# Kernel tuning notes

Hardware: AMD Instinct MI355X
Metric: run time of the kernel (lower is better)

## Reference

```python
import jax, jax.numpy as jnp
import numpy as np

NHEAD = 8
NEG_INF = -1e9
LN_EPS = 1e-5


def setup_inputs() -> dict:
    key = jax.random.key(0)
    ks = jax.random.split(key, 8)
    B, Q, N, C = 2, 256, 16384, 256
    return {
        "queries": jax.random.normal(ks[0], (B, Q, C), jnp.float32),
        "vid_features": jax.random.normal(ks[1], (B, C, N), jnp.float32),
        "vid_mask": jax.random.uniform(ks[2], (B, Q, N), jnp.float32),
        "pos_embed": jax.random.normal(ks[3], (B, C, N), jnp.float32),
        "query_embed": jax.random.normal(ks[4], (B, Q, C), jnp.float32),
        "in_proj_w": jax.random.normal(ks[5], (3 * C, C), jnp.float32) * 0.02,
        "in_proj_b": jnp.zeros((3 * C,), jnp.float32),
        "out_proj_w": jax.random.normal(ks[6], (C, C), jnp.float32) * 0.02,
        "out_proj_b": jnp.zeros((C,), jnp.float32),
        "ln_gamma": jnp.ones((C,), jnp.float32),
        "ln_beta": jnp.zeros((C,), jnp.float32),
    }


def reference(queries, vid_features, vid_mask, pos_embed, query_embed,
              in_proj_w, in_proj_b, out_proj_w, out_proj_b, ln_gamma, ln_beta):
    B, Q, C = queries.shape
    H = NHEAD
    d = C // H

    vf = jnp.transpose(vid_features, (0, 2, 1))   # B N C
    pe = jnp.transpose(pos_embed, (0, 2, 1))      # B N C

    q_in = queries + query_embed                  # with_pos_embed on queries
    k_in = vf + pe                                # with_pos_embed on keys
    v_in = vf

    wq, wk, wv = jnp.split(in_proj_w, 3, axis=0)
    bq, bk, bv = jnp.split(in_proj_b, 3)

    q = (q_in @ wq.T + bq).reshape(B, Q, H, d)
    k = (k_in @ wk.T + bk).reshape(B, -1, H, d)
    v = (v_in @ wv.T + bv).reshape(B, -1, H, d)

    scale = 1.0 / jnp.sqrt(jnp.asarray(d, q.dtype))
    logits = jnp.einsum('bqhd,bnhd->bhqn', q, k) * scale  # B H Q N

    # Hard masking: block keys where mask prob < 0.5; if a query row is
    # fully blocked, fall back to unmasked attention (avoid NaN softmax).
    blocked = vid_mask < 0.5                                 # B Q N
    all_blocked = jnp.all(blocked, axis=-1, keepdims=True)   # B Q 1
    blocked = blocked & jnp.logical_not(all_blocked)
    logits = jnp.where(blocked[:, None, :, :], NEG_INF, logits)

    attn = jax.nn.softmax(logits, axis=-1)
    ctx = jnp.einsum('bhqn,bnhd->bqhd', attn, v).reshape(B, Q, C)
    tgt2 = ctx @ out_proj_w.T + out_proj_b

    # residual + LayerNorm (dropout p=0.0 -> identity)
    x = queries + tgt2
    mu = jnp.mean(x, axis=-1, keepdims=True)
    var = jnp.mean(jnp.square(x - mu), axis=-1, keepdims=True)
    return (x - mu) / jnp.sqrt(var + LN_EPS) * ln_gamma + ln_beta
```

## Files before the change

kernel.cpp:

```cpp
#include <hip/hip_runtime.h>
#include <stdint.h>

#define B_ 2
#define Q_ 256
#define N_ 16384
#define C_ 256
#define H_ 8
#define D_ 32
#define NC_ 32
#define SCALE 0.17677669529663687f

typedef __bf16 bf16x8 __attribute__((ext_vector_type(8)));
typedef float f32x4 __attribute__((ext_vector_type(4)));

__device__ __forceinline__ uint16_t bfbits(float f) {
  union { __bf16 h; uint16_t u; } c;
  c.h = (__bf16)f;
  return c.u;
}
__device__ __forceinline__ uint16_t f2bf(float f) {
  union { float f; uint32_t u; } c; c.f = f;
  uint32_t r = c.u + 0x7FFFu + ((c.u >> 16) & 1u);
  return (uint16_t)(r >> 16);
}
__device__ __forceinline__ uint32_t pk2(float a, float b) {
  return (uint32_t)f2bf(a) | ((uint32_t)f2bf(b) << 16);
}
__device__ __forceinline__ void lgkm0_barrier() {
  __builtin_amdgcn_sched_barrier(0);
  asm volatile("s_waitcnt lgkmcnt(0)" ::: "memory");
  __builtin_amdgcn_sched_barrier(0);
  __builtin_amdgcn_s_barrier();
  __builtin_amdgcn_sched_barrier(0);
}

__global__ __launch_bounds__(256) void prep(const float* __restrict__ inw,
                                            const float* __restrict__ outw,
                                            const float* __restrict__ vm,
                                            uint16_t* __restrict__ wb,
                                            float* __restrict__ woT,
                                            uint32_t* __restrict__ mb) {
  __shared__ __align__(16) char sh[4352];
  const int bid = blockIdx.x;
  const int t = threadIdx.x;
  if (bid < 96) {
    const int i = (bid * 256 + t) * 8;
    const float4 a = *reinterpret_cast<const float4*>(inw + i);
    const float4 b = *reinterpret_cast<const float4*>(inw + i + 4);
    ushort4 lo = {bfbits(a.x), bfbits(a.y), bfbits(a.z), bfbits(a.w)};
    ushort4 hi = {bfbits(b.x), bfbits(b.y), bfbits(b.z), bfbits(b.w)};
    *reinterpret_cast<ushort4*>(wb + i) = lo;
    *reinterpret_cast<ushort4*>(wb + i + 4) = hi;
  } else if (bid < 160) {
    float(*s)[33] = reinterpret_cast<float(*)[33]>(sh);
    const int bb = bid - 96;
    const int bx = bb & 7, by = bb >> 3;
    const int r0 = by * 32, c0 = bx * 32;
    const int tr = t >> 5, tc = t & 31;
#pragma unroll
    for (int k = 0; k < 4; ++k)
      s[tr + 8 * k][tc] = outw[(size_t)(r0 + tr + 8 * k) * 256 + c0 + tc];
    __syncthreads();
#pragma unroll
    for (int k = 0; k < 4; ++k)
      woT[(size_t)(c0 + tr + 8 * k) * 256 + r0 + tc] = s[tc][tr + 8 * k];
  } else {
    uint8_t(*nib)[256] = reinterpret_cast<uint8_t(*)[256]>(sh);
    __shared__ int wcnt[4];
    __shared__ int tot;
    const int bq = bid - 160;
    const float* row = vm + (size_t)bq * N_;
    const int lane = t & 63;
    int cnt = 0;
#pragma unroll
    for (int i = 0; i < 16; ++i) {
      const float4 v = *reinterpret_cast<const float4*>(&row[i * 1024 + 4 * t]);
      const uint32_t nb = (v.x < 0.5f ? 1u : 0u) | (v.y < 0.5f ? 2u : 0u) |
                          (v.z < 0.5f ? 4u : 0u) | (v.w < 0.5f ? 8u : 0u);
      nib[i][t] = (uint8_t)nb;
      cnt += __popc(nb);
    }
    for (int o = 32; o > 0; o >>= 1) cnt += __shfl_down(cnt, o, 64);
    if (lane == 0) wcnt[t >> 6] = cnt;
    __syncthreads();
    if (t == 0) tot = wcnt[0] + wcnt[1] + wcnt[2] + wcnt[3];
    __syncthreads();
    const bool allb = (tot == N_);
    uint32_t* dst = mb + (size_t)bq * 512;
#pragma unroll
    for (int k = 0; k < 2; ++k) {
      const int w = k * 256 + t;
      const int i = w >> 5, tw = w & 31;
      const uint2 u = *reinterpret_cast<const uint2*>(&nib[i][8 * tw]);
      uint32_t y0 = u.x & 0x0F0F0F0Fu; y0 = y0 | (y0 >> 4);
      uint32_t y1 = u.y & 0x0F0F0F0Fu; y1 = y1 | (y1 >> 4);
      const uint32_t word = (y0 & 0xFFu) | (((y0 >> 16) & 0xFFu) << 8) |
                            ((y1 & 0xFFu) << 16) | (((y1 >> 16) & 0xFFu) << 24);
      dst[w] = allb ? 0u : word;
    }
  }
}

__global__ __launch_bounds__(512) void kvqproj(const float* __restrict__ vf,
                                               const float* __restrict__ pe,
                                               const float* __restrict__ queries,
                                               const float* __restrict__ qembed,
                                               const uint16_t* __restrict__ wkv,
                                               const float* __restrict__ bias,
                                               uint16_t* __restrict__ Kb,
                                               uint16_t* __restrict__ Vb,
                                               uint16_t* __restrict__ Qb) {
  __shared__ __align__(16) uint16_t lds[8][64][40];
  const int bid = blockIdx.x;
  const int t = threadIdx.x, wid = t >> 6, lane = t & 63;
  const int g = lane >> 4, c15 = lane & 15;

  if (bid < 1024) {
    const int nb = bid & 511, b = bid >> 9;
    const int n0 = nb * 32;
    const int cin = t >> 1, nh = (t & 1) * 16;
    const int s = cin >> 5, cl = cin & 31;
    const float* Xrow = vf + ((size_t)b * C_ + cin) * N_ + n0 + nh;
    const float* Prow = pe + ((size_t)b * C_ + cin) * N_ + n0 + nh;
    float4 xr4[4], pr4[4];
#pragma unroll
    for (int k = 0; k < 4; ++k) xr4[k] = reinterpret_cast<const float4*>(Xrow)[k];
#pragma unroll
    for (int k = 0; k < 4; ++k) pr4[k] = reinterpret_cast<const float4*>(Prow)[k];
    const float* xf = reinterpret_cast<const float*>(xr4);
    const float* pf = reinterpret_cast<const float*>(pr4);
#pragma unroll
    for (int i = 0; i < 16; ++i) {
      const int n = nh + i;
      const int col = cl ^ (8 * ((n >> 3) & 3));
      lds[s][n][col] = bfbits(xf[i] + pf[i]);
      lds[s][32 + n][col] = bfbits(xf[i]);
    }
    lgkm0_barrier();

    const bool isK = wid < 4;
    const int wc = wid & 3;
    const uint16_t* W = wkv + (isK ? 256 * C_ : 512 * C_);
    f32x4 acc[4][2];
    if (isK) {
#pragma unroll
      for (int cf = 0; cf < 4; ++cf) {
        f32x4 iv;
#pragma unroll
        for (int j = 0; j < 4; ++j) iv[j] = bias[256 + wc * 64 + cf * 16 + 4 * g + j];
        acc[cf][0] = iv;
        acc[cf][1] = iv;
      }
    } else {
#pragma unroll
      for (int cf = 0; cf < 4; ++cf) {
        const float bv = bias[512 + wc * 64 + cf * 16 + c15];
        const f32x4 iv = {bv, bv, bv, bv};
        acc[0][cf] = iv;
        acc[1][cf] = iv;
      }
    }
#pragma unroll
    for (int s8 = 0; s8 < 8; ++s8) {
      bf16x8 Wf[4];
#pragma unroll
      for (int cf = 0; cf < 4; ++cf)
        Wf[cf] = *reinterpret_cast<const bf16x8*>(
            W + (size_t)(wc * 64 + cf * 16 + c15) * C_ + s8 * 32 + g * 8);
      if (isK) {
#pragma unroll
        for (int nf = 0; nf < 2; ++nf) {
          const int r = nf * 16 + c15;
          const bf16x8 Bf = *reinterpret_cast<const bf16x8*>(
              &lds[s8][r][8 * (g ^ ((r >> 3) & 3))]);
#pragma unroll
          for (int cf = 0; cf < 4; ++cf)
            acc[cf][nf] = __builtin_amdgcn_mfma_f32_16x16x32_bf16(Wf[cf], Bf, acc[cf][nf], 0, 0, 0);
        }
      } else {
#pragma unroll
        for (int nf = 0; nf < 2; ++nf) {
          const int r = nf * 16 + c15;
          const bf16x8 Af = *reinterpret_cast<const bf16x8*>(
              &lds[s8][32 + r][8 * (g ^ ((r >> 3) & 3))]);
#pragma unroll
          for (int cf = 0; cf < 4; ++cf)
            acc[nf][cf] = __builtin_amdgcn_mfma_f32_16x16x32_bf16(Af, Wf[cf], acc[nf][cf], 0, 0, 0);
        }
      }
    }
    if (isK) {
      uint16_t* Kp = Kb + (size_t)b * N_ * C_;
#pragma unroll
      for (int cf = 0; cf < 4; ++cf)
#pragma unroll
        for (int nf = 0; nf < 2; ++nf) {
          const f32x4 a = acc[cf][nf];
          uint2 pkv;
          pkv.x = pk2(a[0], a[1]);
          pkv.y = pk2(a[2], a[3]);
          *reinterpret_cast<uint2*>(
              &Kp[(size_t)(n0 + nf * 16 + c15) * C_ + wc * 64 + cf * 16 + 4 * g]) = pkv;
        }
    } else {
      uint16_t* Vp = Vb + (size_t)b * C_ * N_;
#pragma unroll
      for (int nf = 0; nf < 2; ++nf)
#pragma unroll
        for (int cf = 0; cf < 4; ++cf) {
          const f32x4 a = acc[nf][cf];
          uint2 pkv;
          pkv.x = pk2(a[0], a[1]);
          pkv.y = pk2(a[2], a[3]);
          *reinterpret_cast<uint2*>(
              &Vp[(size_t)(wc * 64 + cf * 16 + c15) * N_ + n0 + nf * 16 + 4 * g]) = pkv;
        }
    }
  } else {
    const int qb = bid - 1024;
    const int q0g = qb * 64;
    const int b = q0g >> 8, q0 = q0g & 255;
    const int r = t >> 3, c0 = (t & 7) * 32, s = t & 7;
    const float* Qrow = queries + (size_t)(q0g + r) * C_ + c0;
    const float* Erow = qembed + (size_t)(q0g + r) * C_ + c0;
#pragma unroll
    for (int ph = 0; ph < 2; ++ph) {
      float4 a4[4], e4[4];
#pragma unroll
      for (int k = 0; k < 4; ++k) a4[k] = reinterpret_cast<const float4*>(Qrow + ph * 16)[k];
#pragma unroll
      for (int k = 0; k < 4; ++k) e4[k] = reinterpret_cast<const float4*>(Erow + ph * 16)[k];
      const float* af = reinterpret_cast<const float*>(a4);
      const float* ef = reinterpret_cast<const float*>(e4);
#pragma unroll
      for (int i = 0; i < 16; ++i) {
        const int cl = ph * 16 + i;
        const int col = cl ^ (8 * ((r >> 3) & 3));
        lds[s][r][col] = bfbits(af[i] + ef[i]);
      }
      __builtin_amdgcn_sched_barrier(0);
    }
    lgkm0_barrier();

    const int w = wid;
    f32x4 acc[4][2];
#pragma unroll
    for (int nf = 0; nf < 2; ++nf) {
      const float bv = bias[w * 32 + nf * 16 + c15];
      const f32x4 iv = {bv, bv, bv, bv};
#pragma unroll
      for (int qf = 0; qf < 4; ++qf) acc[qf][nf] = iv;
    }
#pragma unroll
    for (int s8 = 0; s8 < 8; ++s8) {
      bf16x8 Bf[2];
#pragma unroll
      for (int nf = 0; nf < 2; ++nf)
        Bf[nf] = *reinterpret_cast<const bf16x8*>(
            wkv + (size_t)(w * 32 + nf * 16 + c15) * C_ + s8 * 32 + g * 8);
#pragma unroll
      for (int qf = 0; qf < 4; ++qf) {
        const int rr = qf * 16 + c15;
        const bf16x8 Af = *reinterpret_cast<const bf16x8*>(
            &lds[s8][rr][8 * (g ^ ((rr >> 3) & 3))]);
#pragma unroll
        for (int nf = 0; nf < 2; ++nf)
          acc[qf][nf] = __builtin_amdgcn_mfma_f32_16x16x32_bf16(Af, Bf[nf], acc[qf][nf], 0, 0, 0);
      }
    }
#pragma unroll
    for (int qf = 0; qf < 4; ++qf)
#pragma unroll
      for (int nf = 0; nf < 2; ++nf)
#pragma unroll
        for (int j = 0; j < 4; ++j) {
          const int q = q0 + qf * 16 + 4 * g + j;
          const int dk = nf * 16 + c15;
          Qb[((size_t)(b * H_ + w) * Q_ + q) * D_ + dk] = f2bf(acc[qf][nf][j] * SCALE);
        }
  }
}

__global__ __launch_bounds__(512) void attn(const uint16_t* __restrict__ Qb,
                                            const uint16_t* __restrict__ Kb,
                                            const uint16_t* __restrict__ Vb,
                                            const uint32_t* __restrict__ mb,
                                            float* __restrict__ ctx_part,
                                            float* __restrict__ lsum_part) {
  const int bid = blockIdx.x;
  const int nc = bid & 31, h = (bid >> 5) & 7, b = bid >> 8;
  const int t = threadIdx.x, wid = t >> 6, lane = t & 63;
  const int g = lane >> 4, c15 = lane & 15;
  const int qw0 = wid * 32;
  const int nbase = nc * (N_ / NC_);
  constexpr int SS = (N_ / NC_) / 128;

  __shared__ __align__(16) uint16_t kst[2][128][40];
  __shared__ __align__(16) uint16_t vst[2][32][136];
  __shared__ __align__(16) uint16_t plds[8][32][40];

  const uint16_t* Qp = Qb + (size_t)(b * H_ + h) * Q_ * D_;
  bf16x8 qfr[2];
#pragma unroll
  for (int qf = 0; qf < 2; ++qf)
    qfr[qf] = *reinterpret_cast<const bf16x8*>(Qp + (size_t)(qw0 + qf * 16 + c15) * D_ + g * 8);

  f32x4 acc[2][2];
  const f32x4 zero4 = {0.f, 0.f, 0.f, 0.f};
#pragma unroll
  for (int qf = 0; qf < 2; ++qf)
#pragma unroll
    for (int dvf = 0; dvf < 2; ++dvf) acc[qf][dvf] = zero4;
  float lsum[2][4] = {};

  const uint32_t* mrow = mb + (size_t)b * Q_ * (N_ / 32);

  const int krow = t >> 2, kch = t & 3;
  const uint16_t* ksrc = Kb + ((size_t)(b * N_ + nbase + krow)) * C_ + h * D_ + kch * 8;
  const int vrow = t >> 4, vch = t & 15;
  const uint16_t* vsrc = Vb + ((size_t)(b * C_ + h * D_ + vrow)) * N_ + nbase + vch * 8;

  uint4 kreg = *(const uint4*)ksrc;
  uint4 vreg = *(const uint4*)vsrc;

  int cur = 0;
  for (int ss = 0; ss < SS; ++ss) {
    *(uint4*)&kst[cur][krow][kch * 8] = kreg;
    *(uint4*)&vst[cur][vrow][vch * 8] = vreg;
    if (ss < SS - 1) {
      kreg = *(const uint4*)(ksrc + (size_t)(ss + 1) * 128 * C_);
      vreg = *(const uint4*)(vsrc + (ss + 1) * 128);
    }
    lgkm0_barrier();

    const int nstart = nbase + ss * 128;
#pragma unroll
    for (int half = 0; half < 2; ++half) {
      uint32_t mw[2][4][2];
#pragma unroll
      for (int qf = 0; qf < 2; ++qf)
#pragma unroll
        for (int j = 0; j < 4; ++j) {
          const int q = qw0 + qf * 16 + 4 * g + j;
          const uint2 u = *reinterpret_cast<const uint2*>(
              &mrow[(size_t)q * (N_ / 32) + (nstart >> 5) + half * 2]);
          mw[qf][j][0] = u.x;
          mw[qf][j][1] = u.y;
        }
#pragma unroll
      for (int s2 = 0; s2 < 2; ++s2) {
        const int sub = half * 2 + s2;
        const int nl0 = sub * 32;
        bf16x8 kfr[2];
#pragma unroll
        for (int nf = 0; nf < 2; ++nf)
          kfr[nf] = *reinterpret_cast<const bf16x8*>(&kst[cur][nl0 + nf * 16 + c15][g * 8]);
        f32x4 s[2][2];
#pragma unroll
        for (int qf = 0; qf < 2; ++qf)
#pragma unroll
          for (int nf = 0; nf < 2; ++nf)
            s[qf][nf] = __builtin_amdgcn_mfma_f32_16x16x32_bf16(qfr[qf], kfr[nf], zero4, 0, 0, 0);

#pragma unroll
        for (int qf = 0; qf < 2; ++qf) {
#pragma unroll
          for (int j = 0; j < 4; ++j) {
            const uint32_t wmask = mw[qf][j][s2];
#pragma unroll
            for (int nf = 0; nf < 2; ++nf) {
              const int bit = nf * 16 + c15;
              const float p = ((wmask >> bit) & 1u) ? 0.0f : __expf(s[qf][nf][j]);
              lsum[qf][j] += p;
              plds[wid][qf * 16 + 4 * g + j][nf * 16 + c15] = f2bf(p);
            }
          }
        }
        __asm__ volatile("s_waitcnt lgkmcnt(0)" ::: "memory");
#pragma unroll
        for (int qf = 0; qf < 2; ++qf) {
          const bf16x8 pa = *reinterpret_cast<const bf16x8*>(&plds[wid][qf * 16 + c15][g * 8]);
#pragma unroll
          for (int dvf = 0; dvf < 2; ++dvf) {
            const bf16x8 vb =
                *reinterpret_cast<const bf16x8*>(&vst[cur][dvf * 16 + c15][nl0 + g * 8]);
            acc[qf][dvf] = __builtin_amdgcn_mfma_f32_16x16x32_bf16(pa, vb, acc[qf][dvf], 0, 0, 0);
          }
        }
      }
    }
    __builtin_amdgcn_sched_barrier(0);
    cur ^= 1;
  }

#pragma unroll
  for (int qf = 0; qf < 2; ++qf)
#pragma unroll
    for (int j = 0; j < 4; ++j) {
      float v = lsum[qf][j];
      v += __shfl_xor(v, 1, 64);
      v += __shfl_xor(v, 2, 64);
      v += __shfl_xor(v, 4, 64);
      v += __shfl_xor(v, 8, 64);
      lsum[qf][j] = v;
    }

  float* cp = ctx_part + ((size_t)(b * H_ + h) * NC_ + nc) * Q_ * D_;
#pragma unroll
  for (int qf = 0; qf < 2; ++qf)
#pragma unroll
    for (int dvf = 0; dvf < 2; ++dvf)
#pragma unroll
      for (int j = 0; j < 4; ++j) {
        const int q = qw0 + qf * 16 + 4 * g + j;
        cp[(size_t)q * D_ + dvf * 16 + c15] = acc[qf][dvf][j];
      }
  if (c15 == 0) {
    float* lp = lsum_part + ((size_t)(b * H_ + h) * NC_ + nc) * Q_;
#pragma unroll
    for (int qf = 0; qf < 2; ++qf)
#pragma unroll
      for (int j = 0; j < 4; ++j) lp[qw0 + qf * 16 + 4 * g + j] = lsum[qf][j];
  }
}

__global__ __launch_bounds__(256) void epilogue(const float* __restrict__ ctx_part,
                                                const float* __restrict__ lsum_part,
                                                const float* __restrict__ queries,
                                                const float* __restrict__ woT,
                                                const float* __restrict__ bo,
                                                const float* __restrict__ gamma,
                                                const float* __restrict__ beta,
                                                float* __restrict__ out) {
  const int bq = blockIdx.x;
  const int b = bq >> 8, q = bq & 255;
  const int t = threadIdx.x;
  const int h = t >> 5, dv = t & 31;
  float cs = 0.f, ls = 0.f;
  for (int k = 0; k < NC_; ++k) {
    cs += ctx_part[(((size_t)(b * H_ + h) * NC_ + k) * Q_ + q) * D_ + dv];
    ls += lsum_part[((size_t)(b * H_ + h) * NC_ + k) * Q_ + q];
  }
  __shared__ float ctxrow[C_];
  ctxrow[t] = cs / ls;
  __syncthreads();
  float acc = bo[t];
#pragma unroll 8
  for (int j = 0; j < C_; ++j) acc = fmaf(ctxrow[j], woT[(size_t)j * C_ + t], acc);
  const float x = queries[(size_t)bq * C_ + t] + acc;
  float s1 = x, s2 = x * x;
  for (int o = 32; o > 0; o >>= 1) {
    s1 += __shfl_down(s1, o, 64);
    s2 += __shfl_down(s2, o, 64);
  }
  __shared__ float r1[4], r2[4];
  if ((t & 63) == 0) { r1[t >> 6] = s1; r2[t >> 6] = s2; }
  __syncthreads();
  const float mu = (r1[0] + r1[1] + r1[2] + r1[3]) * (1.0f / C_);
  const float e2 = (r2[0] + r2[1] + r2[2] + r2[3]) * (1.0f / C_);
  const float var = e2 - mu * mu;
  out[(size_t)bq * C_ + t] = (x - mu) * rsqrtf(var + 1e-5f) * gamma[t] + beta[t];
}

extern "C" void kernel_launch(void* const* d_in, const int* in_sizes, int n_in,
                              void* d_out, int out_size, void* d_ws, size_t ws_size,
                              hipStream_t stream) {
  const float* queries    = (const float*)d_in[0];
  const float* vidfeat    = (const float*)d_in[1];
  const float* vidmask    = (const float*)d_in[2];
  const float* posembed   = (const float*)d_in[3];
  const float* queryembed = (const float*)d_in[4];
  const float* inw        = (const float*)d_in[5];
  const float* inb        = (const float*)d_in[6];
  const float* outw       = (const float*)d_in[7];
  const float* outb       = (const float*)d_in[8];
  const float* gamma      = (const float*)d_in[9];
  const float* beta       = (const float*)d_in[10];
  float* out = (float*)d_out;

  char* ws = (char*)d_ws;
  size_t off = 0;
  uint16_t* Qb = (uint16_t*)(ws + off); off += (size_t)B_ * H_ * Q_ * D_ * 2;
  uint16_t* Kb = (uint16_t*)(ws + off); off += (size_t)B_ * N_ * C_ * 2;
  uint16_t* Vb = (uint16_t*)(ws + off); off += (size_t)B_ * C_ * N_ * 2;
  uint32_t* mb = (uint32_t*)(ws + off); off += (size_t)B_ * Q_ * (N_ / 32) * 4;
  float* ctxp  = (float*)(ws + off);    off += (size_t)B_ * H_ * NC_ * Q_ * D_ * 4;
  float* lsump = (float*)(ws + off);    off += (size_t)B_ * H_ * NC_ * Q_ * 4;
  uint16_t* wkv = (uint16_t*)(ws + off); off += (size_t)768 * C_ * 2;
  float* woT   = (float*)(ws + off);    off += (size_t)C_ * C_ * 4;

  prep<<<dim3(672), dim3(256), 0, stream>>>(inw, outw, vidmask, wkv, woT, mb);
  kvqproj<<<dim3(1032), dim3(512), 0, stream>>>(vidfeat, posembed, queries, queryembed,
                                                wkv, inb, Kb, Vb, Qb);
  attn<<<dim3(B_ * H_ * NC_), dim3(512), 0, stream>>>(Qb, Kb, Vb, mb, ctxp, lsump);
  epilogue<<<dim3(B_ * Q_), dim3(256), 0, stream>>>(ctxp, lsump, queries, woT, outb, gamma, beta, out);
}
```

Baseline: 111.5 us.

## Make K/V projection persistent with register-resident weights and double-buffered LDS staging

The K/V projection drops from 1024 blocks to 256 persistent blocks that each handle four 32-column tiles. Each wave holds its weight slice in registers for the whole kernel instead of reloading it every tile. The next tile's video and pos-embed data is fetched from global memory while the current tile's MFMAs run, using two LDS buffers with a new XOR swizzle. In exchange, the heavy register use (launch_bounds 512,1) lowers occupancy and leaves fewer blocks to hide latency, and the global loads are now strided scalar reads rather than float4.

```diff
diff --git a/kernel.cpp b/kernel.cpp
--- a/kernel.cpp
+++ b/kernel.cpp
@@ -101,123 +101,176 @@
   }
 }
 
-__global__ __launch_bounds__(512) void kvqproj(const float* __restrict__ vf,
-                                               const float* __restrict__ pe,
-                                               const float* __restrict__ queries,
-                                               const float* __restrict__ qembed,
-                                               const uint16_t* __restrict__ wkv,
-                                               const float* __restrict__ bias,
-                                               uint16_t* __restrict__ Kb,
-                                               uint16_t* __restrict__ Vb,
-                                               uint16_t* __restrict__ Qb) {
-  __shared__ __align__(16) uint16_t lds[8][64][40];
+__global__ __launch_bounds__(512, 1) void kvqproj(const float* __restrict__ vf,
+                                                  const float* __restrict__ pe,
+                                                  const float* __restrict__ queries,
+                                                  const float* __restrict__ qembed,
+                                                  const uint16_t* __restrict__ wkv,
+                                                  const float* __restrict__ bias,
+                                                  uint16_t* __restrict__ Kb,
+                                                  uint16_t* __restrict__ Vb,
+                                                  uint16_t* __restrict__ Qb) {
   const int bid = blockIdx.x;
   const int t = threadIdx.x, wid = t >> 6, lane = t & 63;
   const int g = lane >> 4, c15 = lane & 15;
 
-  if (bid < 1024) {
-    const int nb = bid & 511, b = bid >> 9;
-    const int n0 = nb * 32;
-    const int cin = t >> 1, nh = (t & 1) * 16;
-    const int s = cin >> 5, cl = cin & 31;
-    const float* Xrow = vf + ((size_t)b * C_ + cin) * N_ + n0 + nh;
-    const float* Prow = pe + ((size_t)b * C_ + cin) * N_ + n0 + nh;
-    float4 xr4[4], pr4[4];
-#pragma unroll
-    for (int k = 0; k < 4; ++k) xr4[k] = reinterpret_cast<const float4*>(Xrow)[k];
-#pragma unroll
-    for (int k = 0; k < 4; ++k) pr4[k] = reinterpret_cast<const float4*>(Prow)[k];
-    const float* xf = reinterpret_cast<const float*>(xr4);
-    const float* pf = reinterpret_cast<const float*>(pr4);
-#pragma unroll
-    for (int i = 0; i < 16; ++i) {
-      const int n = nh + i;
-      const int col = cl ^ (8 * ((n >> 3) & 3));
-      lds[s][n][col] = bfbits(xf[i] + pf[i]);
-      lds[s][32 + n][col] = bfbits(xf[i]);
-    }
-    lgkm0_barrier();
+  if (bid < 256) {
+    __shared__ __align__(16) uint16_t XPs[2][32][256];
+    __shared__ __align__(16) uint16_t XVs[2][32][256];
+    char* xpb[2] = {(char*)&XPs[0][0][0], (char*)&XPs[1][0][0]};
+    char* xvb[2] = {(char*)&XVs[0][0][0], (char*)&XVs[1][0][0]};
 
     const bool isK = wid < 4;
     const int wc = wid & 3;
-    const uint16_t* W = wkv + (isK ? 256 * C_ : 512 * C_);
-    f32x4 acc[4][2];
-    if (isK) {
-#pragma unroll
-      for (int cf = 0; cf < 4; ++cf) {
-        f32x4 iv;
-#pragma unroll
-        for (int j = 0; j < 4; ++j) iv[j] = bias[256 + wc * 64 + cf * 16 + 4 * g + j];
-        acc[cf][0] = iv;
-        acc[cf][1] = iv;
+
+    const uint16_t* Wbase = wkv + (isK ? 256 * C_ : 512 * C_) + (size_t)(wc * 64 + c15) * C_;
+    bf16x8 Wreg[4][8];
+#pragma unroll
+    for (int cf = 0; cf < 4; ++cf)
+#pragma unroll
+      for (int s8 = 0; s8 < 8; ++s8)
+        Wreg[cf][s8] = *reinterpret_cast<const bf16x8*>(Wbase + (size_t)cf * 16 * C_ + s8 * 32 + g * 8);
+
+    f32x4 bk4[4];
+    float bv4[4];
+#pragma unroll
+    for (int cf = 0; cf < 4; ++cf) {
+      if (isK) {
+#pragma unroll
+        for (int j = 0; j < 4; ++j) bk4[cf][j] = bias[256 + wc * 64 + cf * 16 + 4 * g + j];
+      } else {
+        bv4[cf] = bias[512 + wc * 64 + cf * 16 + c15];
       }
-    } else {
-#pragma unroll
-      for (int cf = 0; cf < 4; ++cf) {
-        const float bv = bias[512 + wc * 64 + cf * 16 + c15];
-        const f32x4 iv = {bv, bv, bv, bv};
-        acc[0][cf] = iv;
-        acc[1][cf] = iv;
-      }
-    }
-#pragma unroll
-    for (int s8 = 0; s8 < 8; ++s8) {
-      bf16x8 Wf[4];
-#pragma unroll
-      for (int cf = 0; cf < 4; ++cf)
-        Wf[cf] = *reinterpret_cast<const bf16x8*>(
-            W + (size_t)(wc * 64 + cf * 16 + c15) * C_ + s8 * 32 + g * 8);
-      if (isK) {
-#pragma unroll
-        for (int nf = 0; nf < 2; ++nf) {
-          const int r = nf * 16 + c15;
-          const bf16x8 Bf = *reinterpret_cast<const bf16x8*>(
-              &lds[s8][r][8 * (g ^ ((r >> 3) & 3))]);
-#pragma unroll
-          for (int cf = 0; cf < 4; ++cf)
-            acc[cf][nf] = __builtin_amdgcn_mfma_f32_16x16x32_bf16(Wf[cf], Bf, acc[cf][nf], 0, 0, 0);
-        }
-      } else {
-#pragma unroll
-        for (int nf = 0; nf < 2; ++nf) {
-          const int r = nf * 16 + c15;
-          const bf16x8 Af = *reinterpret_cast<const bf16x8*>(
-              &lds[s8][32 + r][8 * (g ^ ((r >> 3) & 3))]);
-#pragma unroll
-          for (int cf = 0; cf < 4; ++cf)
-            acc[nf][cf] = __builtin_amdgcn_mfma_f32_16x16x32_bf16(Af, Wf[cf], acc[nf][cf], 0, 0, 0);
-        }
-      }
-    }
-    if (isK) {
-      uint16_t* Kp = Kb + (size_t)b * N_ * C_;
-#pragma unroll
-      for (int cf = 0; cf < 4; ++cf)
-#pragma unroll
-        for (int nf = 0; nf < 2; ++nf) {
-          const f32x4 a = acc[cf][nf];
-          uint2 pkv;
-          pkv.x = pk2(a[0], a[1]);
-          pkv.y = pk2(a[2], a[3]);
-          *reinterpret_cast<uint2*>(
-              &Kp[(size_t)(n0 + nf * 16 + c15) * C_ + wc * 64 + cf * 16 + 4 * g]) = pkv;
-        }
-    } else {
-      uint16_t* Vp = Vb + (size_t)b * C_ * N_;
-#pragma unroll
-      for (int nf = 0; nf < 2; ++nf)
-#pragma unroll
-        for (int cf = 0; cf < 4; ++cf) {
-          const f32x4 a = acc[nf][cf];
-          uint2 pkv;
-          pkv.x = pk2(a[0], a[1]);
-          pkv.y = pk2(a[2], a[3]);
-          *reinterpret_cast<uint2*>(
-              &Vp[(size_t)(wc * 64 + cf * 16 + c15) * N_ + n0 + nf * 16 + 4 * g]) = pkv;
-        }
-    }
+    }
+
+    const int sn = t & 31;
+    const int qi = t >> 5;
+    const int swz = ((sn << 1) & 31) << 4;
+    const int g0 = bid * 4;
+
+    float xr[4][4], pr[4][4];
+    f32x4 acc[8];
+
+#define STAGE_LOAD(G)                                                        \
+    {                                                                        \
+      const int b_ = (G) >> 9;                                               \
+      const int n0_ = ((G) & 511) * 32;                                      \
+      const float* Xb_ = vf + (size_t)b_ * C_ * N_ + n0_ + sn;               \
+      const float* Pb_ = pe + (size_t)b_ * C_ * N_ + n0_ + sn;               \
+      _Pragma("unroll") for (int q = 0; q < 4; ++q)                          \
+        _Pragma("unroll") for (int j = 0; j < 4; ++j) {                      \
+          const size_t ro_ = (size_t)(q * 64 + qi * 4 + j) * N_;             \
+          xr[q][j] = Xb_[ro_];                                               \
+          pr[q][j] = Pb_[ro_];                                               \
+        }                                                                    \
+    }
+
+#define STAGE_WRITE(buf)                                                     \
+    {                                                                        \
+      _Pragma("unroll") for (int q = 0; q < 4; ++q) {                        \
+        const int cb_ = (q * 64 + qi * 4) * 2;                               \
+        uint2 wxp_, wxv_;                                                    \
+        wxp_.x = pk2(xr[q][0] + pr[q][0], xr[q][1] + pr[q][1]);              \
+        wxp_.y = pk2(xr[q][2] + pr[q][2], xr[q][3] + pr[q][3]);              \
+        wxv_.x = pk2(xr[q][0], xr[q][1]);                                    \
+        wxv_.y = pk2(xr[q][2], xr[q][3]);                                    \
+        *(uint2*)(xpb[buf] + sn * 512 + (cb_ ^ swz)) = wxp_;                 \
+        *(uint2*)(xvb[buf] + sn * 512 + (cb_ ^ swz)) = wxv_;                 \
+      }                                                                      \
+    }
+
+#define ACCINIT()                                                            \
+    {                                                                        \
+      if (isK) {                                                             \
+        _Pragma("unroll") for (int cf = 0; cf < 4; ++cf) {                   \
+          acc[cf * 2 + 0] = bk4[cf];                                         \
+          acc[cf * 2 + 1] = bk4[cf];                                         \
+        }                                                                    \
+      } else {                                                               \
+        _Pragma("unroll") for (int cf = 0; cf < 4; ++cf) {                   \
+          const f32x4 iv_ = {bv4[cf], bv4[cf], bv4[cf], bv4[cf]};            \
+          acc[0 * 4 + cf] = iv_;                                             \
+          acc[1 * 4 + cf] = iv_;                                             \
+        }                                                                    \
+      }                                                                      \
+    }
+
+#define COMPUTE(buf)                                                         \
+    {                                                                        \
+      _Pragma("unroll") for (int s8 = 0; s8 < 8; ++s8)                       \
+        _Pragma("unroll") for (int nf = 0; nf < 2; ++nf) {                   \
+          const int nr_ = nf * 16 + c15;                                     \
+          const int off_ = nr_ * 512 + ((s8 * 64 + g * 16) ^ (((nr_ << 1) & 31) << 4)); \
+          if (isK) {                                                         \
+            const bf16x8 Bf_ = *(const bf16x8*)(xpb[buf] + off_);            \
+            _Pragma("unroll") for (int cf = 0; cf < 4; ++cf)                 \
+              acc[cf * 2 + nf] = __builtin_amdgcn_mfma_f32_16x16x32_bf16(    \
+                  Wreg[cf][s8], Bf_, acc[cf * 2 + nf], 0, 0, 0);             \
+          } else {                                                           \
+            const bf16x8 Af_ = *(const bf16x8*)(xvb[buf] + off_);            \
+            _Pragma("unroll") for (int cf = 0; cf < 4; ++cf)                 \
+              acc[nf * 4 + cf] = __builtin_amdgcn_mfma_f32_16x16x32_bf16(    \
+                  Af_, Wreg[cf][s8], acc[nf * 4 + cf], 0, 0, 0);             \
+          }                                                                  \
+        }                                                                    \
+    }
+
+#define STORE(G)                                                             \
+    {                                                                        \
+      const int b_ = (G) >> 9;                                               \
+      const int n0_ = ((G) & 511) * 32;                                      \
+      if (isK) {                                                             \
+        uint16_t* Kp_ = Kb + (size_t)b_ * N_ * C_;                           \
+        _Pragma("unroll") for (int cf = 0; cf < 4; ++cf)                     \
+          _Pragma("unroll") for (int nf = 0; nf < 2; ++nf) {                 \
+            const f32x4 a_ = acc[cf * 2 + nf];                               \
+            uint2 pkv_;                                                      \
+            pkv_.x = pk2(a_[0], a_[1]);                                      \
+            pkv_.y = pk2(a_[2], a_[3]);                                      \
+            *(uint2*)&Kp_[(size_t)(n0_ + nf * 16 + c15) * C_ + wc * 64 + cf * 16 + 4 * g] = pkv_; \
+          }                                                                  \
+      } else {                                                               \
+        uint16_t* Vp_ = Vb + (size_t)b_ * C_ * N_;                           \
+        _Pragma("unroll") for (int nf = 0; nf < 2; ++nf)                     \
+          _Pragma("unroll") for (int cf = 0; cf < 4; ++cf) {                 \
+            const f32x4 a_ = acc[nf * 4 + cf];                               \
+            uint2 pkv_;                                                      \
+            pkv_.x = pk2(a_[0], a_[1]);                                      \
+            pkv_.y = pk2(a_[2], a_[3]);                                      \
+            *(uint2*)&Vp_[(size_t)(wc * 64 + cf * 16 + c15) * N_ + n0_ + nf * 16 + 4 * g] = pkv_; \
+          }                                                                  \
+      }                                                                      \
+    }
+
+    STAGE_LOAD(g0);
+    STAGE_WRITE(0);
+    STAGE_LOAD(g0 + 1);
+    lgkm0_barrier();
+
+    ACCINIT(); COMPUTE(0); STORE(g0);
+    STAGE_WRITE(1);
+    STAGE_LOAD(g0 + 2);
+    lgkm0_barrier();
+
+    ACCINIT(); COMPUTE(1); STORE(g0 + 1);
+    STAGE_WRITE(0);
+    STAGE_LOAD(g0 + 3);
+    lgkm0_barrier();
+
+    ACCINIT(); COMPUTE(0); STORE(g0 + 2);
+    STAGE_WRITE(1);
+    lgkm0_barrier();
+
+    ACCINIT(); COMPUTE(1); STORE(g0 + 3);
+
+#undef STAGE_LOAD
+#undef STAGE_WRITE
+#undef ACCINIT
+#undef COMPUTE
+#undef STORE
   } else {
-    const int qb = bid - 1024;
+    __shared__ __align__(16) uint16_t qlds[8][64][40];
+    const int qb = bid - 256;
     const int q0g = qb * 64;
     const int b = q0g >> 8, q0 = q0g & 255;
     const int r = t >> 3, c0 = (t & 7) * 32, s = t & 7;
@@ -236,7 +289,7 @@
       for (int i = 0; i < 16; ++i) {
         const int cl = ph * 16 + i;
         const int col = cl ^ (8 * ((r >> 3) & 3));
-        lds[s][r][col] = bfbits(af[i] + ef[i]);
+        qlds[s][r][col] = bfbits(af[i] + ef[i]);
       }
       __builtin_amdgcn_sched_barrier(0);
     }
@@ -262,7 +315,7 @@
       for (int qf = 0; qf < 4; ++qf) {
         const int rr = qf * 16 + c15;
         const bf16x8 Af = *reinterpret_cast<const bf16x8*>(
-            &lds[s8][rr][8 * (g ^ ((rr >> 3) & 3))]);
+            &qlds[s8][rr][8 * (g ^ ((rr >> 3) & 3))]);
 #pragma unroll
         for (int nf = 0; nf < 2; ++nf)
           acc[qf][nf] = __builtin_amdgcn_mfma_f32_16x16x32_bf16(Af, Bf[nf], acc[qf][nf], 0, 0, 0);
@@ -490,8 +543,8 @@
   float* woT   = (float*)(ws + off);    off += (size_t)C_ * C_ * 4;
 
   prep<<<dim3(672), dim3(256), 0, stream>>>(inw, outw, vidmask, wkv, woT, mb);
-  kvqproj<<<dim3(1032), dim3(512), 0, stream>>>(vidfeat, posembed, queries, queryembed,
-                                                wkv, inb, Kb, Vb, Qb);
+  kvqproj<<<dim3(264), dim3(512), 0, stream>>>(vidfeat, posembed, queries, queryembed,
+                                               wkv, inb, Kb, Vb, Qb);
   attn<<<dim3(B_ * H_ * NC_), dim3(512), 0, stream>>>(Qb, Kb, Vb, mb, ctxp, lsump);
   epilogue<<<dim3(B_ * Q_), dim3(256), 0, stream>>>(ctxp, lsump, queries, woT, outb, gamma, beta, out);
 }
```

Result: faster. 108.1 us (-3.0%).

## Enlarge K/V projection tiles and software-pipeline input loads with double-buffered LDS

Applied to the files above, without the earlier changes.

The K/V projection path moves from 1024 blocks of 32 tokens to 256 blocks of 128 tokens. Each wave now holds 32 accumulator fragments, so every weight fragment loaded from global memory is reused across four times as many tokens. The channel loop is split into 8 stages. Each stage prefetches the next video/pos-embed slice and weight fragments into registers while the MFMAs consume the current LDS buffer, using two LDS buffers. The cost is about one block per CU (launch_bounds 512,1) and far fewer waves to hide latency, plus unswizzled column-wise LDS writes that may cause bank conflicts.

```diff
diff --git a/kernel.cpp b/kernel.cpp
--- a/kernel.cpp
+++ b/kernel.cpp
@@ -101,123 +101,158 @@
   }
 }
 
-__global__ __launch_bounds__(512) void kvqproj(const float* __restrict__ vf,
-                                               const float* __restrict__ pe,
-                                               const float* __restrict__ queries,
-                                               const float* __restrict__ qembed,
-                                               const uint16_t* __restrict__ wkv,
-                                               const float* __restrict__ bias,
-                                               uint16_t* __restrict__ Kb,
-                                               uint16_t* __restrict__ Vb,
-                                               uint16_t* __restrict__ Qb) {
-  __shared__ __align__(16) uint16_t lds[8][64][40];
+__global__ __launch_bounds__(512, 1) void kvqproj(const float* __restrict__ vf,
+                                                  const float* __restrict__ pe,
+                                                  const float* __restrict__ queries,
+                                                  const float* __restrict__ qembed,
+                                                  const uint16_t* __restrict__ wkv,
+                                                  const float* __restrict__ bias,
+                                                  uint16_t* __restrict__ Kb,
+                                                  uint16_t* __restrict__ Vb,
+                                                  uint16_t* __restrict__ Qb) {
   const int bid = blockIdx.x;
   const int t = threadIdx.x, wid = t >> 6, lane = t & 63;
   const int g = lane >> 4, c15 = lane & 15;
 
-  if (bid < 1024) {
-    const int nb = bid & 511, b = bid >> 9;
-    const int n0 = nb * 32;
-    const int cin = t >> 1, nh = (t & 1) * 16;
-    const int s = cin >> 5, cl = cin & 31;
-    const float* Xrow = vf + ((size_t)b * C_ + cin) * N_ + n0 + nh;
-    const float* Prow = pe + ((size_t)b * C_ + cin) * N_ + n0 + nh;
-    float4 xr4[4], pr4[4];
-#pragma unroll
-    for (int k = 0; k < 4; ++k) xr4[k] = reinterpret_cast<const float4*>(Xrow)[k];
-#pragma unroll
-    for (int k = 0; k < 4; ++k) pr4[k] = reinterpret_cast<const float4*>(Prow)[k];
-    const float* xf = reinterpret_cast<const float*>(xr4);
-    const float* pf = reinterpret_cast<const float*>(pr4);
-#pragma unroll
-    for (int i = 0; i < 16; ++i) {
-      const int n = nh + i;
-      const int col = cl ^ (8 * ((n >> 3) & 3));
-      lds[s][n][col] = bfbits(xf[i] + pf[i]);
-      lds[s][32 + n][col] = bfbits(xf[i]);
-    }
-    lgkm0_barrier();
-
+  if (bid < 256) {
+    __shared__ __align__(16) uint16_t XP[2][128][34];
+    __shared__ __align__(16) uint16_t XV[2][128][34];
+
+    const int b = bid >> 7, nt = bid & 127;
+    const int n0 = nt * 128;
     const bool isK = wid < 4;
     const int wc = wid & 3;
-    const uint16_t* W = wkv + (isK ? 256 * C_ : 512 * C_);
-    f32x4 acc[4][2];
+    const uint16_t* Wsec = wkv + (isK ? 256 * C_ : 512 * C_) + (size_t)(wc * 64 + c15) * C_;
+
+    f32x4 acc[32];
     if (isK) {
 #pragma unroll
       for (int cf = 0; cf < 4; ++cf) {
         f32x4 iv;
 #pragma unroll
         for (int j = 0; j < 4; ++j) iv[j] = bias[256 + wc * 64 + cf * 16 + 4 * g + j];
-        acc[cf][0] = iv;
-        acc[cf][1] = iv;
+#pragma unroll
+        for (int nf = 0; nf < 8; ++nf) acc[cf * 8 + nf] = iv;
       }
     } else {
 #pragma unroll
       for (int cf = 0; cf < 4; ++cf) {
         const float bv = bias[512 + wc * 64 + cf * 16 + c15];
         const f32x4 iv = {bv, bv, bv, bv};
-        acc[0][cf] = iv;
-        acc[1][cf] = iv;
+#pragma unroll
+        for (int nf = 0; nf < 8; ++nf) acc[nf * 4 + cf] = iv;
       }
     }
-#pragma unroll
-    for (int s8 = 0; s8 < 8; ++s8) {
-      bf16x8 Wf[4];
-#pragma unroll
-      for (int cf = 0; cf < 4; ++cf)
-        Wf[cf] = *reinterpret_cast<const bf16x8*>(
-            W + (size_t)(wc * 64 + cf * 16 + c15) * C_ + s8 * 32 + g * 8);
-      if (isK) {
-#pragma unroll
-        for (int nf = 0; nf < 2; ++nf) {
-          const int r = nf * 16 + c15;
-          const bf16x8 Bf = *reinterpret_cast<const bf16x8*>(
-              &lds[s8][r][8 * (g ^ ((r >> 3) & 3))]);
-#pragma unroll
-          for (int cf = 0; cf < 4; ++cf)
-            acc[cf][nf] = __builtin_amdgcn_mfma_f32_16x16x32_bf16(Wf[cf], Bf, acc[cf][nf], 0, 0, 0);
-        }
-      } else {
-#pragma unroll
-        for (int nf = 0; nf < 2; ++nf) {
-          const int r = nf * 16 + c15;
-          const bf16x8 Af = *reinterpret_cast<const bf16x8*>(
-              &lds[s8][32 + r][8 * (g ^ ((r >> 3) & 3))]);
-#pragma unroll
-          for (int cf = 0; cf < 4; ++cf)
-            acc[nf][cf] = __builtin_amdgcn_mfma_f32_16x16x32_bf16(Af, Wf[cf], acc[nf][cf], 0, 0, 0);
-        }
-      }
-    }
+
+    const int scin = t >> 4, nq = t & 15;
+    const float* Xb = vf + ((size_t)b * C_ + scin) * N_ + n0 + nq * 4;
+    const float* Pb = pe + ((size_t)b * C_ + scin) * N_ + n0 + nq * 4;
+
+    float4 xA[2], pA[2], xB[2], pB[2];
+    bf16x8 Wa[4], Wz[4];
+
+#define LOADW(W, s)                                                          \
+    {                                                                        \
+      _Pragma("unroll") for (int cf = 0; cf < 4; ++cf)                       \
+          W[cf] = *(const bf16x8*)(Wsec + (size_t)cf * 16 * C_ + (s) * 32 + g * 8); \
+    }
+
+#define LOADA(XA, PA, s)                                                     \
+    {                                                                        \
+      _Pragma("unroll") for (int j = 0; j < 2; ++j) {                        \
+        XA[j] = *(const float4*)(Xb + (size_t)(s) * 32 * N_ + j * 64);       \
+        PA[j] = *(const float4*)(Pb + (size_t)(s) * 32 * N_ + j * 64);       \
+      }                                                                      \
+    }
+
+#define WRITEA(XA, PA, buf)                                                  \
+    {                                                                        \
+      _Pragma("unroll") for (int j = 0; j < 2; ++j) {                        \
+        const float* xf_ = (const float*)&XA[j];                             \
+        const float* pf_ = (const float*)&PA[j];                             \
+        _Pragma("unroll") for (int i = 0; i < 4; ++i) {                      \
+          const int n_ = j * 64 + nq * 4 + i;                                \
+          XP[buf][n_][scin] = f2bf(xf_[i] + pf_[i]);                         \
+          XV[buf][n_][scin] = f2bf(xf_[i]);                                  \
+        }                                                                    \
+      }                                                                      \
+    }
+
+#define COMPUTE(W, buf)                                                      \
+    {                                                                        \
+      if (isK) {                                                             \
+        _Pragma("unroll") for (int nf = 0; nf < 8; ++nf) {                   \
+          const int r_ = nf * 16 + c15;                                      \
+          const bf16x8 Bf_ = *(const bf16x8*)&XP[buf][r_][g * 8];            \
+          _Pragma("unroll") for (int cf = 0; cf < 4; ++cf)                   \
+              acc[cf * 8 + nf] = __builtin_amdgcn_mfma_f32_16x16x32_bf16(    \
+                  W[cf], Bf_, acc[cf * 8 + nf], 0, 0, 0);                    \
+        }                                                                    \
+      } else {                                                               \
+        _Pragma("unroll") for (int nf = 0; nf < 8; ++nf) {                   \
+          const int r_ = nf * 16 + c15;                                      \
+          const bf16x8 Af_ = *(const bf16x8*)&XV[buf][r_][g * 8];            \
+          _Pragma("unroll") for (int cf = 0; cf < 4; ++cf)                   \
+              acc[nf * 4 + cf] = __builtin_amdgcn_mfma_f32_16x16x32_bf16(    \
+                  Af_, W[cf], acc[nf * 4 + cf], 0, 0, 0);                    \
+        }                                                                    \
+      }                                                                      \
+    }
+
+    LOADW(Wa, 0);
+    LOADA(xA, pA, 0);
+    LOADA(xB, pB, 1);
+
+    LOADW(Wz, 1); WRITEA(xA, pA, 0); LOADA(xA, pA, 2);
+    lgkm0_barrier(); COMPUTE(Wa, 0); __builtin_amdgcn_sched_barrier(0);
+    LOADW(Wa, 2); WRITEA(xB, pB, 1); LOADA(xB, pB, 3);
+    lgkm0_barrier(); COMPUTE(Wz, 1); __builtin_amdgcn_sched_barrier(0);
+    LOADW(Wz, 3); WRITEA(xA, pA, 0); LOADA(xA, pA, 4);
+    lgkm0_barrier(); COMPUTE(Wa, 0); __builtin_amdgcn_sched_barrier(0);
+    LOADW(Wa, 4); WRITEA(xB, pB, 1); LOADA(xB, pB, 5);
+    lgkm0_barrier(); COMPUTE(Wz, 1); __builtin_amdgcn_sched_barrier(0);
+    LOADW(Wz, 5); WRITEA(xA, pA, 0); LOADA(xA, pA, 6);
+    lgkm0_barrier(); COMPUTE(Wa, 0); __builtin_amdgcn_sched_barrier(0);
+    LOADW(Wa, 6); WRITEA(xB, pB, 1); LOADA(xB, pB, 7);
+    lgkm0_barrier(); COMPUTE(Wz, 1); __builtin_amdgcn_sched_barrier(0);
+    LOADW(Wz, 7); WRITEA(xA, pA, 0);
+    lgkm0_barrier(); COMPUTE(Wa, 0); __builtin_amdgcn_sched_barrier(0);
+    WRITEA(xB, pB, 1);
+    lgkm0_barrier(); COMPUTE(Wz, 1); __builtin_amdgcn_sched_barrier(0);
+
+#undef LOADW
+#undef LOADA
+#undef WRITEA
+#undef COMPUTE
+
     if (isK) {
       uint16_t* Kp = Kb + (size_t)b * N_ * C_;
 #pragma unroll
       for (int cf = 0; cf < 4; ++cf)
 #pragma unroll
-        for (int nf = 0; nf < 2; ++nf) {
-          const f32x4 a = acc[cf][nf];
+        for (int nf = 0; nf < 8; ++nf) {
+          const f32x4 a = acc[cf * 8 + nf];
           uint2 pkv;
           pkv.x = pk2(a[0], a[1]);
           pkv.y = pk2(a[2], a[3]);
-          *reinterpret_cast<uint2*>(
-              &Kp[(size_t)(n0 + nf * 16 + c15) * C_ + wc * 64 + cf * 16 + 4 * g]) = pkv;
+          *(uint2*)&Kp[(size_t)(n0 + nf * 16 + c15) * C_ + wc * 64 + cf * 16 + 4 * g] = pkv;
         }
     } else {
       uint16_t* Vp = Vb + (size_t)b * C_ * N_;
 #pragma unroll
-      for (int nf = 0; nf < 2; ++nf)
+      for (int nf = 0; nf < 8; ++nf)
 #pragma unroll
         for (int cf = 0; cf < 4; ++cf) {
-          const f32x4 a = acc[nf][cf];
+          const f32x4 a = acc[nf * 4 + cf];
           uint2 pkv;
           pkv.x = pk2(a[0], a[1]);
           pkv.y = pk2(a[2], a[3]);
-          *reinterpret_cast<uint2*>(
-              &Vp[(size_t)(wc * 64 + cf * 16 + c15) * N_ + n0 + nf * 16 + 4 * g]) = pkv;
+          *(uint2*)&Vp[(size_t)(wc * 64 + cf * 16 + c15) * N_ + n0 + nf * 16 + 4 * g] = pkv;
         }
     }
   } else {
-    const int qb = bid - 1024;
+    __shared__ __align__(16) uint16_t qlds[8][64][40];
+    const int qb = bid - 256;
     const int q0g = qb * 64;
     const int b = q0g >> 8, q0 = q0g & 255;
     const int r = t >> 3, c0 = (t & 7) * 32, s = t & 7;
@@ -236,7 +271,7 @@
       for (int i = 0; i < 16; ++i) {
         const int cl = ph * 16 + i;
         const int col = cl ^ (8 * ((r >> 3) & 3));
-        lds[s][r][col] = bfbits(af[i] + ef[i]);
+        qlds[s][r][col] = bfbits(af[i] + ef[i]);
       }
       __builtin_amdgcn_sched_barrier(0);
     }
@@ -262,7 +297,7 @@
       for (int qf = 0; qf < 4; ++qf) {
         const int rr = qf * 16 + c15;
         const bf16x8 Af = *reinterpret_cast<const bf16x8*>(
-            &lds[s8][rr][8 * (g ^ ((rr >> 3) & 3))]);
+            &qlds[s8][rr][8 * (g ^ ((rr >> 3) & 3))]);
 #pragma unroll
         for (int nf = 0; nf < 2; ++nf)
           acc[qf][nf] = __builtin_amdgcn_mfma_f32_16x16x32_bf16(Af, Bf[nf], acc[qf][nf], 0, 0, 0);
@@ -490,8 +525,8 @@
   float* woT   = (float*)(ws + off);    off += (size_t)C_ * C_ * 4;
 
   prep<<<dim3(672), dim3(256), 0, stream>>>(inw, outw, vidmask, wkv, woT, mb);
-  kvqproj<<<dim3(1032), dim3(512), 0, stream>>>(vidfeat, posembed, queries, queryembed,
-                                                wkv, inb, Kb, Vb, Qb);
+  kvqproj<<<dim3(264), dim3(512), 0, stream>>>(vidfeat, posembed, queries, queryembed,
+                                               wkv, inb, Kb, Vb, Qb);
   attn<<<dim3(B_ * H_ * NC_), dim3(512), 0, stream>>>(Qb, Kb, Vb, mb, ctxp, lsump);
   epilogue<<<dim3(B_ * Q_), dim3(256), 0, stream>>>(ctxp, lsump, queries, woT, outb, gamma, beta, out);
 }
```

After: 152.1 us. 36.5% more time.
